# Performance work log

Measured on AMD Instinct MI355X. Metric: run time of the kernel, lower is better.

Reference implementation:

```python
import jax, jax.numpy as jnp
import numpy as np

B, N, E = 2, 20000, 160000
D, U = 1, 100          # input_dim, num_units
IN = D + U             # 101
NEG_SLOPE = 0.2        # PyG GATv2Conv default


def setup_inputs() -> dict:
    key = jax.random.key(0)
    ks = jax.random.split(key, 20)
    s = 0.1
    inp = {
        "inputs": jax.random.normal(ks[0], (B, N * D), jnp.float32),
        "state": jax.random.normal(ks[1], (B, N * U), jnp.float32),
        "src": jax.random.randint(ks[2], (E,), 0, N),
        "dst": jax.random.randint(ks[3], (E,), 0, N),
        # GATv2Conv(101, 200) params: lin_l, lin_r, att, out-bias
        "Wl1": jax.random.normal(ks[4], (IN, 2 * U), jnp.float32) * s,
        "bl1": jax.random.normal(ks[5], (2 * U,), jnp.float32) * s,
        "Wr1": jax.random.normal(ks[6], (IN, 2 * U), jnp.float32) * s,
        "br1": jax.random.normal(ks[7], (2 * U,), jnp.float32) * s,
        "att1": jax.random.normal(ks[8], (2 * U,), jnp.float32) * s,
        "bg1": jax.random.normal(ks[9], (2 * U,), jnp.float32) * s,
        "bias0": jax.random.normal(ks[10], (2 * U,), jnp.float32) * s,
        # GATv2Conv(101, 100) params
        "Wl2": jax.random.normal(ks[11], (IN, U), jnp.float32) * s,
        "bl2": jax.random.normal(ks[12], (U,), jnp.float32) * s,
        "Wr2": jax.random.normal(ks[13], (IN, U), jnp.float32) * s,
        "br2": jax.random.normal(ks[14], (U,), jnp.float32) * s,
        "att2": jax.random.normal(ks[15], (U,), jnp.float32) * s,
        "bg2": jax.random.normal(ks[16], (U,), jnp.float32) * s,
        "bias1": jax.random.normal(ks[17], (U,), jnp.float32) * s,
    }
    return inp


def _gatv2(x, src_f, dst_f, Wl, bl, Wr, br, att, bg):
    # x: (B, N, IN); edges (with self-loops) flow src -> dst.
    xl = x @ Wl + bl                                   # (B, N, C) source transform
    xr = x @ Wr + br                                   # (B, N, C) target transform
    msg = jax.nn.leaky_relu(xl[:, src_f] + xr[:, dst_f], NEG_SLOPE)  # (B, Ef, C)
    e = jnp.einsum('bec,c->be', msg, att)              # (B, Ef) attention logits
    seg_max = jax.vmap(lambda v: jax.ops.segment_max(v, dst_f, num_segments=N))(e)
    ea = jnp.exp(e - seg_max[:, dst_f])
    denom = jax.vmap(lambda v: jax.ops.segment_sum(v, dst_f, num_segments=N))(ea)
    alpha = ea / denom[:, dst_f]                       # per-target softmax
    out = jax.vmap(
        lambda a, xs: jax.ops.segment_sum(a[:, None] * xs, dst_f, num_segments=N)
    )(alpha, xl[:, src_f])                             # (B, N, C)
    return out + bg


def reference(inputs, state, src, dst,
              Wl1, bl1, Wr1, br1, att1, bg1, bias0,
              Wl2, bl2, Wr2, br2, att2, bg2, bias1):
    loops = jnp.arange(N)
    src_f = jnp.concatenate([src, loops])              # PyG adds self-loops
    dst_f = jnp.concatenate([dst, loops])
    inputs3 = inputs.reshape(B, N, D)
    state3 = state.reshape(B, N, U)

    # _gc1: GATv2(101 -> 200) + bias_0, sigmoid gates r, u
    xs = jnp.concatenate([inputs3, state3], axis=2)    # (B, N, 101)
    g1 = _gatv2(xs, src_f, dst_f, Wl1, bl1, Wr1, br1, att1, bg1) + bias0
    val = jax.nn.sigmoid(g1)                           # (B, N, 200)
    r = val[..., :U].reshape(B, N * U)
    u = val[..., U:].reshape(B, N * U)

    # _gc2: GATv2(101 -> 100) on [inputs, r*state] + bias_1, tanh
    xs2 = jnp.concatenate([inputs3, (r * state).reshape(B, N, U)], axis=2)
    c = jnp.tanh(_gatv2(xs2, src_f, dst_f, Wl2, bl2, Wr2, br2, att2, bg2) + bias1)
    c = c.reshape(B, N * U)

    new_state = u * state + (1.0 - u) * c              # (B, N*U)
    return new_state
```

## Files before the change

kernel.cpp:

```cpp
#include <hip/hip_runtime.h>
#include <stdint.h>

typedef __attribute__((ext_vector_type(8))) short short8;
typedef __attribute__((ext_vector_type(4))) short short4v;
typedef __attribute__((ext_vector_type(4))) float f32x4;

static constexpr int BB = 2, NN = 20000, UU = 100;
static constexpr int MT = BB * NN;
static constexpr int MPAD = 40064;
static constexpr int GB1 = 313;
static constexpr float NEG = 0.2f;

__device__ __forceinline__ float b2f(short s) {
  union { uint32_t u; float f; } cv; cv.u = ((uint32_t)(uint16_t)s) << 16; return cv.f;
}
__device__ __forceinline__ short f2b(float x) {
  union { float f; uint32_t u; } cv; cv.f = x;
  uint32_t r = cv.u + 0x7FFFu + ((cv.u >> 16) & 1u);
  return (short)(r >> 16);
}

template<int CTRL>
__device__ __forceinline__ float dppadd(float x) {
  int v = __builtin_amdgcn_update_dpp(0, __float_as_int(x), CTRL, 0xF, 0xF, false);
  return x + __int_as_float(v);
}
__device__ __forceinline__ float red32(float x) {
  x = dppadd<0x121>(x);
  x = dppadd<0x122>(x);
  x = dppadd<0x124>(x);
  x = dppadd<0x128>(x);
  return x + __shfl_xor(x, 16);
}

#define GL2LDS(gsrc, ldst)                                                          \
  __builtin_amdgcn_global_load_lds((const __attribute__((address_space(1))) void*)(gsrc), \
                                   (__attribute__((address_space(3))) void*)(ldst), 16, 0, 0)


__global__ void k_prep(const float* __restrict__ inp, const float* __restrict__ st,
                       const float* __restrict__ Wl1, const float* __restrict__ Wr1,
                       const float* __restrict__ Wl2, const float* __restrict__ Wr2,
                       short* __restrict__ A, short* __restrict__ BT1,
                       short* __restrict__ BT2, int* __restrict__ cursor) {
  int t = blockIdx.x * 256 + threadIdx.x;
  if (t < MT * 16) {
    int r = t >> 4, g = t & 15;
    short8 v;
#pragma unroll
    for (int j = 0; j < 8; ++j) {
      int e = g * 8 + j;
      float x = 0.f;
      if (e == 0) x = inp[r];
      else if (e <= 100) x = st[(size_t)r * 100 + e - 1];
      v[j] = f2b(x);
    }
    *(short8*)(A + (size_t)r * 128 + ((g ^ (r & 7)) << 3)) = v;
  }
  if (t < 512 * 16) {
    int n = t >> 4, g = t & 15;
    short8 v;
#pragma unroll
    for (int j = 0; j < 8; ++j) {
      int k = g * 8 + j;
      float x = 0.f;
      if (k < 101 && n < 400)
        x = (n < 200) ? Wl1[(size_t)k * 200 + n] : Wr1[(size_t)k * 200 + n - 200];
      v[j] = f2b(x);
    }
    *(short8*)(BT1 + (size_t)n * 128 + ((g ^ (n & 7)) << 3)) = v;
  }
  if (t < 256 * 16) {
    int n = t >> 4, g = t & 15;
    short8 v;
#pragma unroll
    for (int j = 0; j < 8; ++j) {
      int k = g * 8 + j;
      int ksrc = (k < 100) ? k + 1 : ((k == 100) ? 0 : -1);
      float x = 0.f;
      if (ksrc >= 0 && n < 200)
        x = (n < 100) ? Wl2[(size_t)ksrc * 100 + n] : Wr2[(size_t)ksrc * 100 + n - 100];
      v[j] = f2b(x);
    }
    *(short8*)(BT2 + (size_t)n * 128 + ((g ^ (n & 7)) << 3)) = v;
  }
  if (t < NN) cursor[t] = 0;
}


__global__ __launch_bounds__(1024) void k_scan(int* __restrict__ histcur,
                                               int* __restrict__ rowptr, int N, int E) {
  __shared__ int part[1024];
  int t = threadIdx.x;
  int CH = (N + 1023) / 1024;
  int beg = t * CH; if (beg > N) beg = N;
  int end = beg + CH; if (end > N) end = N;
  int s = 0;
  for (int i = beg; i < end; ++i) s += histcur[i];
  part[t] = s;
  __syncthreads();
  for (int off = 1; off < 1024; off <<= 1) {
    int v = (t >= off) ? part[t - off] : 0;
    __syncthreads();
    part[t] += v;
    __syncthreads();
  }
  int base = (t == 0) ? 0 : part[t - 1];
  for (int i = beg; i < end; ++i) {
    int h = histcur[i];
    rowptr[i] = base;
    histcur[i] = base;
    base += h;
  }
  if (t == 1023) rowptr[N] = part[1023];
}

__global__ void k_scatter(const int* __restrict__ src, const int* __restrict__ dst, int E,
                          int* __restrict__ cursor, int* __restrict__ col) {
  int e = blockIdx.x * 256 + threadIdx.x;
  if (e < E) {
    int p = atomicAdd(&cursor[dst[e]], 1);
    col[p] = src[e];
  }
}


template<int NOUT, int SPLIT>
__global__ __launch_bounds__(256) void k_gemm(
    const short* __restrict__ A, const short* __restrict__ BT,
    const float* __restrict__ bias_l, const float* __restrict__ bias_r,
    short* __restrict__ X, int nbg,
    const int* __restrict__ dstE, int E, int* __restrict__ hist) {
  __shared__ __align__(16) short As[128 * 128];
  __shared__ __align__(16) short Bs[128 * 128];
  int tid = threadIdx.x;
  if ((int)blockIdx.x >= nbg) {
    int e = (blockIdx.x - nbg) * 256 + tid;
    if (e < E) atomicAdd(&hist[dstE[e]], 1);
    return;
  }
  int m0 = (blockIdx.x % GB1) * 128;
  int n0 = (blockIdx.x / GB1) * 128;
  {
    const short* gA = A + (size_t)m0 * 128;
    const short* gB = BT + (size_t)n0 * 128;
#pragma unroll
    for (int i = 0; i < 8; ++i) {
      GL2LDS(gA + i * 2048 + tid * 8, As + i * 2048 + tid * 8);
      GL2LDS(gB + i * 2048 + tid * 8, Bs + i * 2048 + tid * 8);
    }
  }
  __syncthreads();

  int wv = tid >> 6, lane = tid & 63;
  int m_off = (wv & 1) * 64, n_off = (wv >> 1) * 64;
  int lrow = lane & 15, lk = lane >> 4;
  f32x4 acc[4][4];
#pragma unroll
  for (int i = 0; i < 4; ++i)
#pragma unroll
    for (int j = 0; j < 4; ++j) acc[i][j] = (f32x4){0.f, 0.f, 0.f, 0.f};

#pragma unroll
  for (int kk = 0; kk < 4; ++kk) {
    int g = kk * 4 + lk;
    short8 a[4], b[4];
#pragma unroll
    for (int f = 0; f < 4; ++f) {
      int ra = m_off + f * 16 + lrow;
      a[f] = *(const short8*)(As + ra * 128 + ((g ^ (ra & 7)) << 3));
      int rb = n_off + f * 16 + lrow;
      b[f] = *(const short8*)(Bs + rb * 128 + ((g ^ (rb & 7)) << 3));
    }
#pragma unroll
    for (int i = 0; i < 4; ++i)
#pragma unroll
      for (int j = 0; j < 4; ++j)
        acc[i][j] = __builtin_amdgcn_mfma_f32_16x16x32_bf16(a[i], b[j], acc[i][j], 0, 0, 0);
  }

#pragma unroll
  for (int j = 0; j < 4; ++j) {
    int nc = n0 + n_off + j * 16 + lrow;
    bool nok = nc < NOUT;
    float bv = 0.f;
    int coff = 0;
    if (nok) {
      bv   = (nc < SPLIT) ? bias_l[nc] : bias_r[nc - SPLIT];
      coff = (nc < SPLIT) ? nc : 2 * SPLIT + (nc - SPLIT);
    }
#pragma unroll
    for (int i = 0; i < 4; ++i) {
      int mb = m0 + m_off + i * 16 + lk * 4;
#pragma unroll
      for (int r = 0; r < 4; ++r) {
        int m = mb + r;
        if (nok && m < MT) {
          int b_   = (m >= NN) ? 1 : 0;
          int node = m - b_ * NN;
          X[(size_t)node * (4 * SPLIT) + coff + b_ * SPLIT] = f2b(acc[i][j][r] + bv);
        }
      }
    }
  }
}


#define EDGE1(S, NUM, DEN, NCH, STRIDE)                                            \
  { short8 v_ = *(const short8*)(xb + (size_t)(S) * STRIDE);                       \
    float e_ = 0.f;                                                                \
    _Pragma("unroll") for (int q = 0; q < NCH; ++q) {                              \
      float x_ = b2f(v_[q]); float m_ = x_ + xrv[q];                               \
      m_ = (m_ > 0.f) ? m_ : NEG * m_; e_ = fmaf(m_, attv[q], e_); }               \
    e_ = red32(e_);                                                                \
    float p_ = __expf(e_); DEN += p_;                                              \
    _Pragma("unroll") for (int q = 0; q < NCH; ++q)                                \
      NUM[q] = fmaf(p_, b2f(v_[q]), NUM[q]); }

__global__ __launch_bounds__(256) void k_agg1(
    const short* __restrict__ X1, const int* __restrict__ rowptr, const int* __restrict__ col,
    const float* __restrict__ att, const float* __restrict__ bgv, const float* __restrict__ bias0,
    const float* __restrict__ st, const float* __restrict__ inp,
    short* __restrict__ A2, float* __restrict__ uu) {
  int w = threadIdx.x >> 6, lane = threadIdx.x & 63;
  int n = blockIdx.x * 4 + w;
  if (n >= NN) return;
  int half = lane >> 5, ll = lane & 31;
  int c0 = (ll < 25 ? ll : 24) * 8;
  int idx = half * NN + n;
  const short* xb = X1 + (size_t)half * 200 + c0;

  float attv[8], xrv[8], num[8];
  {
    f32x4 a0 = (f32x4){0,0,0,0}, a1 = (f32x4){0,0,0,0};
    if (ll < 25) { a0 = *(const f32x4*)(att + c0); a1 = *(const f32x4*)(att + c0 + 4); }
#pragma unroll
    for (int q = 0; q < 4; ++q) { attv[q] = a0[q]; attv[4 + q] = a1[q]; }
    short8 xr8 = *(const short8*)(X1 + (size_t)n * 800 + 400 + half * 200 + c0);
#pragma unroll
    for (int q = 0; q < 8; ++q) xrv[q] = (ll < 25) ? b2f(xr8[q]) : 0.f;
  }
  float denom;
  {
    short8 v = *(const short8*)(xb + (size_t)n * 800);
    float xs[8], e = 0.f;
#pragma unroll
    for (int q = 0; q < 8; ++q) {
      xs[q] = b2f(v[q]);
      float msg = xs[q] + xrv[q];
      msg = (msg > 0.f) ? msg : NEG * msg;
      e = fmaf(msg, attv[q], e);
    }
    e = red32(e);
    float pe = __expf(e);
    denom = pe;
#pragma unroll
    for (int q = 0; q < 8; ++q) num[q] = pe * xs[q];
  }

  int beg = rowptr[n], end = rowptr[n + 1];
  int deg = end - beg;
  int degc = min(deg, 64);
  int cv = 0;
  if (deg > 0) cv = col[beg + (lane < degc ? lane : 0)];
  int p = 0;
  for (; p + 2 <= degc; p += 2) {
    int s0 = __shfl(cv, p), s1 = __shfl(cv, p + 1);
    short8 v0 = *(const short8*)(xb + (size_t)s0 * 800);
    short8 v1 = *(const short8*)(xb + (size_t)s1 * 800);
    float e0 = 0.f, e1 = 0.f;
#pragma unroll
    for (int q = 0; q < 8; ++q) {
      float x, m_;
      x = b2f(v0[q]); m_ = x + xrv[q]; m_ = (m_ > 0.f) ? m_ : NEG * m_; e0 = fmaf(m_, attv[q], e0);
      x = b2f(v1[q]); m_ = x + xrv[q]; m_ = (m_ > 0.f) ? m_ : NEG * m_; e1 = fmaf(m_, attv[q], e1);
    }
    e0 = red32(e0); e1 = red32(e1);
    float pe0 = __expf(e0), pe1 = __expf(e1);
    denom += pe0 + pe1;
#pragma unroll
    for (int q = 0; q < 8; ++q)
      num[q] = fmaf(pe1, b2f(v1[q]), fmaf(pe0, b2f(v0[q]), num[q]));
  }
  if (p < degc) {
    int s0 = __shfl(cv, p);
    EDGE1(s0, num, denom, 8, 800);
  }
  for (int t = 64; t < deg; ++t) { int s = col[beg + t]; EDGE1(s, num, denom, 8, 800); }

  float invd = 1.f / denom;
  if (ll < 25) {
    f32x4 g0 = *(const f32x4*)(bgv + c0),   g1 = *(const f32x4*)(bgv + c0 + 4);
    f32x4 h0 = *(const f32x4*)(bias0 + c0), h1 = *(const f32x4*)(bias0 + c0 + 4);
    float vq[8];
#pragma unroll
    for (int q = 0; q < 4; ++q) {
      float o0 = fmaf(num[q], invd, g0[q] + h0[q]);
      vq[q] = 1.f / (1.f + __expf(-o0));
      float o1 = fmaf(num[4 + q], invd, g1[q] + h1[q]);
      vq[4 + q] = 1.f / (1.f + __expf(-o1));
    }
    size_t sb = (size_t)idx * UU;
    if (ll < 12) {
      f32x4 s0 = *(const f32x4*)(st + sb + c0), s1 = *(const f32x4*)(st + sb + c0 + 4);
      short8 wv;
#pragma unroll
      for (int q = 0; q < 4; ++q) { wv[q] = f2b(vq[q] * s0[q]); wv[4 + q] = f2b(vq[4 + q] * s1[q]); }
      *(short8*)(A2 + (size_t)idx * 128 + ((ll ^ (idx & 7)) << 3)) = wv;
    } else if (ll == 12) {
      f32x4 s0 = *(const f32x4*)(st + sb + 96);
      short8 wv;
#pragma unroll
      for (int q = 0; q < 4; ++q) wv[q] = f2b(vq[q] * s0[q]);
      wv[4] = f2b(inp[idx]); wv[5] = 0; wv[6] = 0; wv[7] = 0;
      *(short8*)(A2 + (size_t)idx * 128 + ((12 ^ (idx & 7)) << 3)) = wv;
      *(f32x4*)(uu + sb) = (f32x4){vq[4], vq[5], vq[6], vq[7]};
    } else {
      int uo = c0 - 100;
      *(f32x4*)(uu + sb + uo)     = (f32x4){vq[0], vq[1], vq[2], vq[3]};
      *(f32x4*)(uu + sb + uo + 4) = (f32x4){vq[4], vq[5], vq[6], vq[7]};
      if (ll < 16) {
        short8 z = (short8){0,0,0,0,0,0,0,0};
        *(short8*)(A2 + (size_t)idx * 128 + ((ll ^ (idx & 7)) << 3)) = z;
      }
    }
  }
}

__global__ __launch_bounds__(256) void k_agg2(
    const short* __restrict__ X2, const int* __restrict__ rowptr, const int* __restrict__ col,
    const float* __restrict__ att, const float* __restrict__ bgv, const float* __restrict__ bias1,
    const float* __restrict__ st, float* __restrict__ out) {
  int w = threadIdx.x >> 6, lane = threadIdx.x & 63;
  int n = blockIdx.x * 4 + w;
  if (n >= NN) return;
  int half = lane >> 5, ll = lane & 31;
  int c0 = (ll < 25 ? ll : 24) * 4;
  int idx = half * NN + n;
  const short* xb = X2 + (size_t)half * 100 + c0;

  float attv[4], xrv[4], num[4];
  {
    f32x4 a0 = (f32x4){0,0,0,0};
    if (ll < 25) a0 = *(const f32x4*)(att + c0);
#pragma unroll
    for (int q = 0; q < 4; ++q) attv[q] = a0[q];
    short4v xr4 = *(const short4v*)(X2 + (size_t)n * 400 + 200 + half * 100 + c0);
#pragma unroll
    for (int q = 0; q < 4; ++q) xrv[q] = (ll < 25) ? b2f(xr4[q]) : 0.f;
  }
  float denom;
  {
    short4v v = *(const short4v*)(xb + (size_t)n * 400);
    float xs[4], e = 0.f;
#pragma unroll
    for (int q = 0; q < 4; ++q) {
      xs[q] = b2f(v[q]);
      float msg = xs[q] + xrv[q];
      msg = (msg > 0.f) ? msg : NEG * msg;
      e = fmaf(msg, attv[q], e);
    }
    e = red32(e);
    float pe = __expf(e);
    denom = pe;
#pragma unroll
    for (int q = 0; q < 4; ++q) num[q] = pe * xs[q];
  }

  int beg = rowptr[n], end = rowptr[n + 1];
  int deg = end - beg;
  int degc = min(deg, 64);
  int cv = 0;
  if (deg > 0) cv = col[beg + (lane < degc ? lane : 0)];
  int p = 0;
  for (; p + 2 <= degc; p += 2) {
    int s0 = __shfl(cv, p), s1 = __shfl(cv, p + 1);
    short4v v0 = *(const short4v*)(xb + (size_t)s0 * 400);
    short4v v1 = *(const short4v*)(xb + (size_t)s1 * 400);
    float e0 = 0.f, e1 = 0.f;
#pragma unroll
    for (int q = 0; q < 4; ++q) {
      float x, m_;
      x = b2f(v0[q]); m_ = x + xrv[q]; m_ = (m_ > 0.f) ? m_ : NEG * m_; e0 = fmaf(m_, attv[q], e0);
      x = b2f(v1[q]); m_ = x + xrv[q]; m_ = (m_ > 0.f) ? m_ : NEG * m_; e1 = fmaf(m_, attv[q], e1);
    }
    e0 = red32(e0); e1 = red32(e1);
    float pe0 = __expf(e0), pe1 = __expf(e1);
    denom += pe0 + pe1;
#pragma unroll
    for (int q = 0; q < 4; ++q)
      num[q] = fmaf(pe1, b2f(v1[q]), fmaf(pe0, b2f(v0[q]), num[q]));
  }
  if (p < degc) {
    int s0 = __shfl(cv, p);
    { short4v v_ = *(const short4v*)(xb + (size_t)s0 * 400);
      float e_ = 0.f;
#pragma unroll
      for (int q = 0; q < 4; ++q) {
        float x_ = b2f(v_[q]); float m_ = x_ + xrv[q];
        m_ = (m_ > 0.f) ? m_ : NEG * m_; e_ = fmaf(m_, attv[q], e_);
      }
      e_ = red32(e_);
      float p_ = __expf(e_); denom += p_;
#pragma unroll
      for (int q = 0; q < 4; ++q) num[q] = fmaf(p_, b2f(v_[q]), num[q]);
    }
  }
  for (int t = 64; t < deg; ++t) {
    int s = col[beg + t];
    { short4v v_ = *(const short4v*)(xb + (size_t)s * 400);
      float e_ = 0.f;
#pragma unroll
      for (int q = 0; q < 4; ++q) {
        float x_ = b2f(v_[q]); float m_ = x_ + xrv[q];
        m_ = (m_ > 0.f) ? m_ : NEG * m_; e_ = fmaf(m_, attv[q], e_);
      }
      e_ = red32(e_);
      float p_ = __expf(e_); denom += p_;
#pragma unroll
      for (int q = 0; q < 4; ++q) num[q] = fmaf(p_, b2f(v_[q]), num[q]);
    }
  }

  float invd = 1.f / denom;
  if (ll < 25) {
    f32x4 g0 = *(const f32x4*)(bgv + c0);
    f32x4 h0 = *(const f32x4*)(bias1 + c0);
    size_t sb = (size_t)idx * UU;
    f32x4 uv = *(const f32x4*)(out + sb + c0);
    f32x4 sv = *(const f32x4*)(st + sb + c0);
    f32x4 res;
#pragma unroll
    for (int q = 0; q < 4; ++q) {
      float o   = fmaf(num[q], invd, g0[q] + h0[q]);
      float cvh = tanhf(o);
      res[q] = uv[q] * sv[q] + (1.f - uv[q]) * cvh;
    }
    *(f32x4*)(out + sb + c0) = res;
  }
}


extern "C" void kernel_launch(void* const* d_in, const int* in_sizes, int n_in,
                              void* d_out, int out_size, void* d_ws, size_t ws_size,
                              hipStream_t stream) {
  const float* inp  = (const float*)d_in[0];
  const float* st   = (const float*)d_in[1];
  const int*   src  = (const int*)d_in[2];
  const int*   dst  = (const int*)d_in[3];
  const float* Wl1  = (const float*)d_in[4];
  const float* bl1  = (const float*)d_in[5];
  const float* Wr1  = (const float*)d_in[6];
  const float* br1  = (const float*)d_in[7];
  const float* att1 = (const float*)d_in[8];
  const float* bg1  = (const float*)d_in[9];
  const float* bias0= (const float*)d_in[10];
  const float* Wl2  = (const float*)d_in[11];
  const float* bl2  = (const float*)d_in[12];
  const float* Wr2  = (const float*)d_in[13];
  const float* br2  = (const float*)d_in[14];
  const float* att2 = (const float*)d_in[15];
  const float* bg2  = (const float*)d_in[16];
  const float* bias1= (const float*)d_in[17];

  const int N = NN;
  const int E = in_sizes[2];

  short* X1  = (short*)d_ws;
  short* X2  = X1;
  short* Aws = X1 + (size_t)NN * 800;
  short* BT1 = Aws + (size_t)MPAD * 128;
  short* BT2 = BT1 + 512 * 128;
  int* rowptr = (int*)(BT2 + 256 * 128);
  int* cursor = rowptr + (N + 1);
  int* col    = cursor + N;

  k_prep<<<(MT * 16 + 255) / 256, 256, 0, stream>>>(inp, st, Wl1, Wr1, Wl2, Wr2,
                                                    Aws, BT1, BT2, cursor);
  {
    int nbg = GB1 * 4;
    int nbh = (E + 255) / 256;
    k_gemm<400, 200><<<nbg + nbh, 256, 0, stream>>>(Aws, BT1, bl1, br1, X1, nbg,
                                                    dst, E, cursor);
  }
  k_scan<<<1, 1024, 0, stream>>>(cursor, rowptr, N, E);
  k_scatter<<<(E + 255) / 256, 256, 0, stream>>>(src, dst, E, cursor, col);
  k_agg1<<<(NN + 3) / 4, 256, 0, stream>>>(X1, rowptr, col, att1, bg1, bias0, st, inp,
                                           Aws, (float*)d_out);
  k_gemm<200, 100><<<GB1 * 2, 256, 0, stream>>>(Aws, BT2, bl2, br2, X2, GB1 * 2,
                                                nullptr, 0, nullptr);
  k_agg2<<<(NN + 3) / 4, 256, 0, stream>>>(X2, rowptr, col, att2, bg2, bias1, st,
                                           (float*)d_out);
}
```

Baseline: 180.6 us.

## Replace LDS-staged GEMM with direct-from-global per-wave 64x64 tiles

Rewrites the MFMA GEMM so each wave loads its A and B fragments straight from global memory into registers, with no LDS staging. The XOR swizzle is removed from all writers of the A/BT buffers to match. The edge histogram, previously fused into the GEMM launch, becomes its own kernel and the GEMM moves after scatter. This drops LDS use and the barrier, but each wave re-reads the B tile with no sharing inside the block and issues strided 16-byte global loads, which leans on the L2 cache for reuse.

```diff
diff --git a/kernel.cpp b/kernel.cpp
--- a/kernel.cpp
+++ b/kernel.cpp
@@ -7,8 +7,7 @@
 
 static constexpr int BB = 2, NN = 20000, UU = 100;
 static constexpr int MT = BB * NN;
-static constexpr int MPAD = 40064;
-static constexpr int GB1 = 313;
+static constexpr int MPAD = 40192;
 static constexpr float NEG = 0.2f;
 
 __device__ __forceinline__ float b2f(short s) {
@@ -32,10 +31,6 @@
   x = dppadd<0x128>(x);
   return x + __shfl_xor(x, 16);
 }
-
-#define GL2LDS(gsrc, ldst)                                                          \
-  __builtin_amdgcn_global_load_lds((const __attribute__((address_space(1))) void*)(gsrc), \
-                                   (__attribute__((address_space(3))) void*)(ldst), 16, 0, 0)
 
 
 __global__ void k_prep(const float* __restrict__ inp, const float* __restrict__ st,
@@ -55,7 +50,7 @@
       else if (e <= 100) x = st[(size_t)r * 100 + e - 1];
       v[j] = f2b(x);
     }
-    *(short8*)(A + (size_t)r * 128 + ((g ^ (r & 7)) << 3)) = v;
+    *(short8*)(A + (size_t)r * 128 + (g << 3)) = v;
   }
   if (t < 512 * 16) {
     int n = t >> 4, g = t & 15;
@@ -68,7 +63,7 @@
         x = (n < 200) ? Wl1[(size_t)k * 200 + n] : Wr1[(size_t)k * 200 + n - 200];
       v[j] = f2b(x);
     }
-    *(short8*)(BT1 + (size_t)n * 128 + ((g ^ (n & 7)) << 3)) = v;
+    *(short8*)(BT1 + (size_t)n * 128 + (g << 3)) = v;
   }
   if (t < 256 * 16) {
     int n = t >> 4, g = t & 15;
@@ -82,11 +77,16 @@
         x = (n < 100) ? Wl2[(size_t)ksrc * 100 + n] : Wr2[(size_t)ksrc * 100 + n - 100];
       v[j] = f2b(x);
     }
-    *(short8*)(BT2 + (size_t)n * 128 + ((g ^ (n & 7)) << 3)) = v;
+    *(short8*)(BT2 + (size_t)n * 128 + (g << 3)) = v;
   }
   if (t < NN) cursor[t] = 0;
 }
 
+
+__global__ void k_hist(const int* __restrict__ dst, int E, int* __restrict__ hist) {
+  int e = blockIdx.x * 256 + threadIdx.x;
+  if (e < E) atomicAdd(&hist[dst[e]], 1);
+}
 
 __global__ __launch_bounds__(1024) void k_scan(int* __restrict__ histcur,
                                                int* __restrict__ rowptr, int N, int E) {
@@ -126,35 +126,17 @@
 
 
 template<int NOUT, int SPLIT>
-__global__ __launch_bounds__(256) void k_gemm(
+__global__ __launch_bounds__(256) void k_gemmd(
     const short* __restrict__ A, const short* __restrict__ BT,
     const float* __restrict__ bias_l, const float* __restrict__ bias_r,
-    short* __restrict__ X, int nbg,
-    const int* __restrict__ dstE, int E, int* __restrict__ hist) {
-  __shared__ __align__(16) short As[128 * 128];
-  __shared__ __align__(16) short Bs[128 * 128];
-  int tid = threadIdx.x;
-  if ((int)blockIdx.x >= nbg) {
-    int e = (blockIdx.x - nbg) * 256 + tid;
-    if (e < E) atomicAdd(&hist[dstE[e]], 1);
-    return;
-  }
-  int m0 = (blockIdx.x % GB1) * 128;
-  int n0 = (blockIdx.x / GB1) * 128;
-  {
-    const short* gA = A + (size_t)m0 * 128;
-    const short* gB = BT + (size_t)n0 * 128;
-#pragma unroll
-    for (int i = 0; i < 8; ++i) {
-      GL2LDS(gA + i * 2048 + tid * 8, As + i * 2048 + tid * 8);
-      GL2LDS(gB + i * 2048 + tid * 8, Bs + i * 2048 + tid * 8);
-    }
-  }
-  __syncthreads();
-
-  int wv = tid >> 6, lane = tid & 63;
-  int m_off = (wv & 1) * 64, n_off = (wv >> 1) * 64;
+    short* __restrict__ X) {
+  int w = threadIdx.x >> 6, lane = threadIdx.x & 63;
+  int m0 = (blockIdx.x * 4 + w) * 64;
+  int n0 = blockIdx.y * 64;
   int lrow = lane & 15, lk = lane >> 4;
+  const short* Ab = A  + ((size_t)m0 + lrow) * 128 + lk * 8;
+  const short* Bb = BT + ((size_t)n0 + lrow) * 128 + lk * 8;
+
   f32x4 acc[4][4];
 #pragma unroll
   for (int i = 0; i < 4; ++i)
@@ -163,14 +145,11 @@
 
 #pragma unroll
   for (int kk = 0; kk < 4; ++kk) {
-    int g = kk * 4 + lk;
     short8 a[4], b[4];
 #pragma unroll
     for (int f = 0; f < 4; ++f) {
-      int ra = m_off + f * 16 + lrow;
-      a[f] = *(const short8*)(As + ra * 128 + ((g ^ (ra & 7)) << 3));
-      int rb = n_off + f * 16 + lrow;
-      b[f] = *(const short8*)(Bs + rb * 128 + ((g ^ (rb & 7)) << 3));
+      a[f] = *(const short8*)(Ab + f * (16 * 128) + kk * 32);
+      b[f] = *(const short8*)(Bb + f * (16 * 128) + kk * 32);
     }
 #pragma unroll
     for (int i = 0; i < 4; ++i)
@@ -181,7 +160,7 @@
 
 #pragma unroll
   for (int j = 0; j < 4; ++j) {
-    int nc = n0 + n_off + j * 16 + lrow;
+    int nc = n0 + j * 16 + lrow;
     bool nok = nc < NOUT;
     float bv = 0.f;
     int coff = 0;
@@ -191,7 +170,7 @@
     }
 #pragma unroll
     for (int i = 0; i < 4; ++i) {
-      int mb = m0 + m_off + i * 16 + lk * 4;
+      int mb = m0 + i * 16 + lk * 4;
 #pragma unroll
       for (int r = 0; r < 4; ++r) {
         int m = mb + r;
@@ -306,14 +285,14 @@
       short8 wv;
 #pragma unroll
       for (int q = 0; q < 4; ++q) { wv[q] = f2b(vq[q] * s0[q]); wv[4 + q] = f2b(vq[4 + q] * s1[q]); }
-      *(short8*)(A2 + (size_t)idx * 128 + ((ll ^ (idx & 7)) << 3)) = wv;
+      *(short8*)(A2 + (size_t)idx * 128 + (ll << 3)) = wv;
     } else if (ll == 12) {
       f32x4 s0 = *(const f32x4*)(st + sb + 96);
       short8 wv;
 #pragma unroll
       for (int q = 0; q < 4; ++q) wv[q] = f2b(vq[q] * s0[q]);
       wv[4] = f2b(inp[idx]); wv[5] = 0; wv[6] = 0; wv[7] = 0;
-      *(short8*)(A2 + (size_t)idx * 128 + ((12 ^ (idx & 7)) << 3)) = wv;
+      *(short8*)(A2 + (size_t)idx * 128 + (12 << 3)) = wv;
       *(f32x4*)(uu + sb) = (f32x4){vq[4], vq[5], vq[6], vq[7]};
     } else {
       int uo = c0 - 100;
@@ -321,7 +300,7 @@
       *(f32x4*)(uu + sb + uo + 4) = (f32x4){vq[4], vq[5], vq[6], vq[7]};
       if (ll < 16) {
         short8 z = (short8){0,0,0,0,0,0,0,0};
-        *(short8*)(A2 + (size_t)idx * 128 + ((ll ^ (idx & 7)) << 3)) = z;
+        *(short8*)(A2 + (size_t)idx * 128 + (ll << 3)) = z;
       }
     }
   }
@@ -477,18 +456,19 @@
 
   k_prep<<<(MT * 16 + 255) / 256, 256, 0, stream>>>(inp, st, Wl1, Wr1, Wl2, Wr2,
                                                     Aws, BT1, BT2, cursor);
-  {
-    int nbg = GB1 * 4;
-    int nbh = (E + 255) / 256;
-    k_gemm<400, 200><<<nbg + nbh, 256, 0, stream>>>(Aws, BT1, bl1, br1, X1, nbg,
-                                                    dst, E, cursor);
-  }
+  k_hist<<<(E + 255) / 256, 256, 0, stream>>>(dst, E, cursor);
   k_scan<<<1, 1024, 0, stream>>>(cursor, rowptr, N, E);
   k_scatter<<<(E + 255) / 256, 256, 0, stream>>>(src, dst, E, cursor, col);
+  {
+    dim3 g(157, 8);
+    k_gemmd<400, 200><<<g, 256, 0, stream>>>(Aws, BT1, bl1, br1, X1);
+  }
   k_agg1<<<(NN + 3) / 4, 256, 0, stream>>>(X1, rowptr, col, att1, bg1, bias0, st, inp,
                                            Aws, (float*)d_out);
-  k_gemm<200, 100><<<GB1 * 2, 256, 0, stream>>>(Aws, BT2, bl2, br2, X2, GB1 * 2,
-                                                nullptr, 0, nullptr);
+  {
+    dim3 g(157, 4);
+    k_gemmd<200, 100><<<g, 256, 0, stream>>>(Aws, BT2, bl2, br2, X2);
+  }
   k_agg2<<<(NN + 3) / 4, 256, 0, stream>>>(X2, rowptr, col, att2, bg2, bias1, st,
                                            (float*)d_out);
 }
```

After: 192.8 us. +6.8%, slower.
